# Kernel tuning notes

Measured on AMD Instinct MI355X. Metric: run time of the kernel, lower is better.

## Reference

```python
import jax, jax.numpy as jnp
import numpy as np

B, S, D_IN, E, H, WIN = 2, 4096, 512, 512, 8, 128
HD = E // H
NEG = -1e30


def setup_inputs() -> dict:
    key = jax.random.key(0)
    k0, k1, k2 = jax.random.split(key, 3)
    x = jax.random.normal(k0, (B, S, D_IN), jnp.float32)
    w_qkv = jax.random.normal(k1, (D_IN, 3 * E), jnp.float32) / np.sqrt(D_IN)
    b_qkv = jnp.zeros((3 * E,), jnp.float32)
    w_o = jax.random.normal(k2, (E, E), jnp.float32) / np.sqrt(E)
    b_o = jnp.zeros((E,), jnp.float32)
    return dict(x=x, w_qkv=w_qkv, b_qkv=b_qkv, w_o=w_o, b_o=b_o)


def _sliding_window_attn(q, k, v, w):
    # q,k,v: (B, S, H, HD). Longformer sliding-chunks: each query attends to
    # keys within +/- w positions (band of 2w+1), out-of-range masked to -inf.
    b, s, h, hd = q.shape
    assert s % (2 * w) == 0
    c = s // w  # number of width-w query chunks
    qc = q.transpose(0, 2, 1, 3).reshape(b, h, c, w, hd)  # (B,H,C,w,HD)

    def windows(t):
        # build per-chunk 3w key/value windows [c*w - w, c*w + 2w)
        t = t.transpose(0, 2, 1, 3)  # (B,H,S,HD)
        t = jnp.pad(t, ((0, 0), (0, 0), (w, w), (0, 0)))
        t = t.reshape(b, h, c + 2, w, hd)
        return jnp.concatenate([t[:, :, 0:c], t[:, :, 1:c + 1], t[:, :, 2:c + 2]], axis=3)  # (B,H,C,3w,HD)

    kc = windows(k)
    vc = windows(v)

    # chunked logits over the 3w window, scaled by sqrt(d_k)
    logits3 = jnp.einsum('bhcxd,bhcyd->bhcxy', qc, kc) / jnp.sqrt(jnp.asarray(hd, q.dtype))

    # extract diagonal band: band[x, r] = logits3[x, x + r], r in [0, 2w]
    row = jnp.arange(w)[:, None]            # (w,1)
    col = row + jnp.arange(2 * w + 1)[None, :]  # (w,2w+1), index into 3w window
    band = logits3[..., row, col]           # (B,H,C,w,2w+1)

    # mask positions outside [0, S): global key j = i + r - w
    i = (jnp.arange(c) * w)[:, None, None] + jnp.arange(w)[None, :, None]  # (C,w,1)
    j = i + (jnp.arange(2 * w + 1) - w)[None, None, :]                      # (C,w,2w+1)
    valid = (j >= 0) & (j < s)
    band = jnp.where(valid, band, NEG)

    probs = jax.nn.softmax(band, axis=-1)  # (B,H,C,w,2w+1)

    # scatter band probs back into the 3w window and contract with values
    probs3 = jnp.zeros_like(logits3).at[..., row, col].set(probs)  # (B,H,C,w,3w)
    out = jnp.einsum('bhcxy,bhcyd->bhcxd', probs3, vc)  # (B,H,C,w,HD)
    return out.reshape(b, h, s, hd).transpose(0, 2, 1, 3)  # (B,S,H,HD)


def reference(x, w_qkv, b_qkv, w_o, b_o):
    bsz, s, _ = x.shape
    qkv = x @ w_qkv + b_qkv                      # (B,S,3E)
    qkv = qkv.reshape(bsz, s, H, 3 * HD)
    q = qkv[..., :HD]
    k = qkv[..., HD:2 * HD]
    v = qkv[..., 2 * HD:]
    vals = _sliding_window_attn(q, k, v, WIN).reshape(bsz, s, E)
    return vals @ w_o + b_o
```

## Files before the change

### kernel.cpp

```cpp
#include <hip/hip_runtime.h>
#include <hip/hip_bf16.h>
#include <math.h>

typedef _Float16 f16;
typedef __attribute__((ext_vector_type(8))) _Float16 f16x8;
typedef __attribute__((ext_vector_type(4))) _Float16 f16x4;
typedef __attribute__((ext_vector_type(4))) float f32x4;

#define S_LEN 4096
#define NHEAD 8
#define HDIM 64
#define EMB 512
#define KDIM 512
#define LOG2E 1.4426950408889634f

#if __has_builtin(__builtin_amdgcn_exp2f)
#define EXP2F(x) __builtin_amdgcn_exp2f(x)
#else
#define EXP2F(x) exp2f(x)
#endif

__device__ __forceinline__ void g2l16(const void* g, void* l) {
  __builtin_amdgcn_global_load_lds(
      reinterpret_cast<const __attribute__((address_space(1))) unsigned int*>(
          reinterpret_cast<uintptr_t>(g)),
      reinterpret_cast<__attribute__((address_space(3))) unsigned int*>(
          static_cast<unsigned int>(reinterpret_cast<uintptr_t>(l))),
      16, 0, 0);
}

__global__ void cast_f32_f16_kernel(const float* __restrict__ in, f16* __restrict__ out, int n) {
  int i = (blockIdx.x * 256 + threadIdx.x) * 4;
  if (i >= n) return;
  float4 v = *(const float4*)(in + i);
  f16x4 o = { (f16)v.x, (f16)v.y, (f16)v.z, (f16)v.w };
  *(f16x4*)(out + i) = o;
}

__global__ void transpose_cast_kernel(const float* __restrict__ in, f16* __restrict__ out, int R, int C) {
  __shared__ f16 tile[64][65];
  const int c0 = blockIdx.x * 64, r0 = blockIdx.y * 64;
  const int tid = threadIdx.x;
#pragma unroll
  for (int i = 0; i < 16; ++i) {
    const int idx = i * 256 + tid;
    const int lr = idx >> 6, lc = idx & 63;
    tile[lr][lc] = (f16)in[(size_t)(r0 + lr) * C + (c0 + lc)];
  }
  __syncthreads();
#pragma unroll
  for (int i = 0; i < 16; ++i) {
    const int idx = i * 256 + tid;
    const int lc = idx >> 6, lr = idx & 63;
    out[(size_t)(c0 + lc) * R + (r0 + lr)] = tile[lr][lc];
  }
}

#define TM 128
#define TK 32

template<int MODE, int TN>
__global__ __launch_bounds__(256) void gemm_bt_kernel(
    const f16* __restrict__ A, const f16* __restrict__ Bt, const float* __restrict__ bias,
    f16* __restrict__ Qo, f16* __restrict__ Ko, f16* __restrict__ Vo,
    float* __restrict__ Co, int M, int N) {
  constexpr int JN = TN / 32;
  constexpr int BCH = TN / 64;
  __shared__ f16 As[TM][TK];
  __shared__ f16 Bs[TN][TK];
  const int m0 = blockIdx.x * TM, n0 = blockIdx.y * TN;
  const int tid = threadIdx.x;
  const int lane = tid & 63, wid = tid >> 6;
  const int wr = wid >> 1, wc = wid & 1;
  const int g = lane >> 4, q16 = lane & 15;

  const int srow = lane >> 2;
  const int skof = (lane & 3) * 8;
  const f16* Ag[2]; char* Al[2];
#pragma unroll
  for (int cb = 0; cb < 2; ++cb) {
    const int ch = wid * 2 + cb;
    Ag[cb] = A + (size_t)(m0 + ch * 16 + srow) * KDIM + skof;
    Al[cb] = (char*)As + ch * 1024;
  }
  const f16* Bg[BCH]; char* Bl[BCH];
#pragma unroll
  for (int cb = 0; cb < BCH; ++cb) {
    const int ch = wid * BCH + cb;
    Bg[cb] = Bt + (size_t)(n0 + ch * 16 + srow) * KDIM + skof;
    Bl[cb] = (char*)Bs + ch * 1024;
  }

  f32x4 zero = {0.f, 0.f, 0.f, 0.f};
  f32x4 acc[4][JN];
#pragma unroll
  for (int i = 0; i < 4; i++)
#pragma unroll
    for (int j = 0; j < JN; j++) acc[i][j] = zero;

  for (int kk = 0; kk < KDIM; kk += TK) {
    g2l16(Ag[0] + kk, Al[0]);
    g2l16(Ag[1] + kk, Al[1]);
#pragma unroll
    for (int cb = 0; cb < BCH; ++cb) g2l16(Bg[cb] + kk, Bl[cb]);
    __syncthreads();
    f16x8 af[4], bfr[JN];
#pragma unroll
    for (int i = 0; i < 4; i++) af[i] = *(const f16x8*)&As[wr * 64 + i * 16 + q16][8 * g];
#pragma unroll
    for (int j = 0; j < JN; j++) bfr[j] = *(const f16x8*)&Bs[wc * (TN / 2) + j * 16 + q16][8 * g];
#pragma unroll
    for (int i = 0; i < 4; i++)
#pragma unroll
      for (int j = 0; j < JN; j++)
        acc[i][j] = __builtin_amdgcn_mfma_f32_16x16x32_f16(af[i], bfr[j], acc[i][j], 0, 0, 0);
    __syncthreads();
  }

#pragma unroll
  for (int i = 0; i < 4; i++)
#pragma unroll
    for (int j = 0; j < JN; j++) {
      const int n = n0 + wc * (TN / 2) + j * 16 + q16;
      const float bs = bias[n];
      const int mbase = m0 + wr * 64 + i * 16 + 4 * g;
      if (MODE == 1) {
#pragma unroll
        for (int r = 0; r < 4; r++) Co[(size_t)(mbase + r) * N + n] = acc[i][j][r] + bs;
      } else {
        const int b = mbase >> 12, s = mbase & (S_LEN - 1);
        const int h = n / 192, rr = n - h * 192;
        const size_t bh = (size_t)b * NHEAD + h;
        if (rr < 64) {
#pragma unroll
          for (int r = 0; r < 4; r++)
            Qo[(bh * S_LEN + s + r) * HDIM + rr] = (f16)((acc[i][j][r] + bs) * 0.125f);
        } else if (rr < 128) {
#pragma unroll
          for (int r = 0; r < 4; r++)
            Ko[(bh * S_LEN + s + r) * HDIM + (rr - 64)] = (f16)(acc[i][j][r] + bs);
        } else {
#pragma unroll
          for (int r = 0; r < 4; r++)
            Vo[(bh * S_LEN + s + r) * HDIM + (rr - 128)] = (f16)(acc[i][j][r] + bs);
        }
      }
    }
}

#define VSOFF 40960

__global__ __launch_bounds__(256) void attn_kernel(
    const f16* __restrict__ Q, const f16* __restrict__ K,
    const f16* __restrict__ V, f16* __restrict__ O) {
  __shared__ __align__(16) char smem[81920];

  const int wg = blockIdx.x;
  const int vv = (wg & 7) * 128 + (wg >> 3);
  const int bh = vv >> 6, qc = vv & 63;
  const int b = bh >> 3, h = bh & 7;
  const int tid = threadIdx.x;
  const int wid = tid >> 6, lane = tid & 63;
  const int g = lane >> 4, q16 = lane & 15;
  const int qb = qc * 64;
  const int wb = qb - 128;
  const int qw = qb + wid * 16;
  const int qg = qw + q16;

  const f16* Kb_g = K + (size_t)bh * S_LEN * HDIM;
  const f16* Vb_g = V + (size_t)bh * S_LEN * HDIM;

#pragma unroll
  for (int rd = 0; rd < 10; ++rd) {
    const int idx = rd * 256 + tid;
    const int r = idx >> 3, sl = idx & 7;
    const int key = min(max(wb + r, 0), S_LEN - 1);
    int4 kvv = *(const int4*)(Kb_g + (size_t)key * HDIM + sl * 8);
    *(int4*)(smem + r * 128 + ((sl ^ (r & 7)) << 4)) = kvv;
  }
#pragma unroll
  for (int rd = 0; rd < 10; ++rd) {
    const int idx = rd * 256 + tid;
    const int r = idx >> 3, c8 = (idx & 7) * 8;
    const int key = min(max(wb + r, 0), S_LEN - 1);
    int4 vvv = *(const int4*)(Vb_g + (size_t)key * HDIM + c8);
    *(int4*)(smem + VSOFF + (c8 >> 4) * 10240 + (r >> 2) * 128 + (r & 3) * 32 + ((c8 & 8) << 1)) = vvv;
  }
  __syncthreads();

  const f16* Qb = Q + ((size_t)bh * S_LEN + qw) * HDIM;
  f16x8 qf0 = *(const f16x8*)(Qb + q16 * HDIM + 8 * g);
  f16x8 qf1 = *(const f16x8*)(Qb + q16 * HDIM + 32 + 8 * g);

  f32x4 zero = {0.f, 0.f, 0.f, 0.f};
  f32x4 o[4];
#pragma unroll
  for (int dt = 0; dt < 4; dt++) o[dt] = zero;
  float m_run = 0.f;
  float l_run = 0.f;

  const unsigned troff = (unsigned)(g * 128 + q16 * 8);

#pragma unroll
  for (int t = 0; t < 9; ++t) {
    const int kAp = wid * 16 + 32 * t;
    const int kBp = kAp + 16;
    const int rrA = kAp + q16;
    const int rrB = kBp + q16;
    f16x8 ka0 = *(const f16x8*)(smem + rrA * 128 + (((g    ) ^ (rrA & 7)) << 4));
    f16x8 ka1 = *(const f16x8*)(smem + rrA * 128 + (((g + 4) ^ (rrA & 7)) << 4));
    f16x8 kb0 = *(const f16x8*)(smem + rrB * 128 + (((g    ) ^ (rrB & 7)) << 4));
    f16x8 kb1 = *(const f16x8*)(smem + rrB * 128 + (((g + 4) ^ (rrB & 7)) << 4));

    f32x4 sA = zero, sB = zero;
    sA = __builtin_amdgcn_mfma_f32_16x16x32_f16(ka0, qf0, sA, 0, 0, 0);
    sA = __builtin_amdgcn_mfma_f32_16x16x32_f16(ka1, qf1, sA, 0, 0, 0);
    sB = __builtin_amdgcn_mfma_f32_16x16x32_f16(kb0, qf0, sB, 0, 0, 0);
    sB = __builtin_amdgcn_mfma_f32_16x16x32_f16(kb1, qf1, sB, 0, 0, 0);

    float sv[8];
    float mx = -INFINITY;
#pragma unroll
    for (int i = 0; i < 4; i++) {
      const int kgA = wb + kAp + 4 * g + i;
      const int kgB = wb + kBp + 4 * g + i;
      const bool okA = ((unsigned)(kgA - qg + 128) <= 256u) && ((unsigned)kgA < S_LEN);
      const bool okB = ((unsigned)(kgB - qg + 128) <= 256u) && ((unsigned)kgB < S_LEN);
      sv[i]     = okA ? sA[i] : -INFINITY;
      sv[i + 4] = okB ? sB[i] : -INFINITY;
      mx = fmaxf(mx, fmaxf(sv[i], sv[i + 4]));
    }

    float pA[4], pB[4];
#pragma unroll
    for (int i = 0; i < 4; i++) {
      pA[i] = EXP2F((sv[i] - m_run) * LOG2E);
      pB[i] = EXP2F((sv[i + 4] - m_run) * LOG2E);
    }

    if (__builtin_expect(!__all(mx - m_run <= 8.f), 0)) {
      float mxq = fmaxf(mx, __shfl_xor(mx, 16));
      mxq = fmaxf(mxq, __shfl_xor(mxq, 32));
      const float mnew = fmaxf(m_run, mxq);
      const float resc = EXP2F((m_run - mnew) * LOG2E);
#pragma unroll
      for (int i = 0; i < 4; i++) { pA[i] *= resc; pB[i] *= resc; }
      l_run *= resc;
      float ri[4];
#pragma unroll
      for (int i = 0; i < 4; i++) ri[i] = __shfl(resc, 4 * g + i);
#pragma unroll
      for (int dt = 0; dt < 4; dt++)
#pragma unroll
        for (int i = 0; i < 4; i++) o[dt][i] *= ri[i];
      m_run = mnew;
    }

    f16x4 pfA, pfB;
#pragma unroll
    for (int i = 0; i < 4; i++) {
      l_run += pA[i] + pB[i];
      pfA[i] = (f16)pA[i];
      pfB[i] = (f16)pB[i];
    }

    const int kcA = kAp;
    const int kcB = min(kBp, 304);
    f16x4 bA[4], bB[4];
#pragma unroll
    for (int dt = 0; dt < 4; ++dt) {
      unsigned aA = (unsigned)(uintptr_t)(smem + VSOFF + dt * 10240 + (kcA >> 2) * 128) + troff;
      unsigned aB = (unsigned)(uintptr_t)(smem + VSOFF + dt * 10240 + (kcB >> 2) * 128) + troff;
      asm volatile("ds_read_b64_tr_b16 %0, %1" : "=v"(bA[dt]) : "v"(aA));
      asm volatile("ds_read_b64_tr_b16 %0, %1" : "=v"(bB[dt]) : "v"(aB));
    }
    asm volatile("s_waitcnt lgkmcnt(0)" ::: "memory");
    __builtin_amdgcn_sched_barrier(0);

#pragma unroll
    for (int dt = 0; dt < 4; dt++) {
      o[dt] = __builtin_amdgcn_mfma_f32_16x16x16f16(pfA, bA[dt], o[dt], 0, 0, 0);
      o[dt] = __builtin_amdgcn_mfma_f32_16x16x16f16(pfB, bB[dt], o[dt], 0, 0, 0);
    }
  }

  l_run += __shfl_xor(l_run, 16);
  l_run += __shfl_xor(l_run, 32);
  const float linv = 1.f / l_run;
  float li[4];
#pragma unroll
  for (int i = 0; i < 4; i++) li[i] = __shfl(linv, 4 * g + i);
#pragma unroll
  for (int dt = 0; dt < 4; dt++)
#pragma unroll
    for (int i = 0; i < 4; i++) {
      const int s_idx = qw + 4 * g + i;
      O[((size_t)b * S_LEN + s_idx) * EMB + h * HDIM + dt * 16 + q16] = (f16)(o[dt][i] * li[i]);
    }
}

extern "C" void kernel_launch(void* const* d_in, const int* in_sizes, int n_in,
                              void* d_out, int out_size, void* d_ws, size_t ws_size,
                              hipStream_t stream) {
  const float* x     = (const float*)d_in[0];
  const float* w_qkv = (const float*)d_in[1];
  const float* b_qkv = (const float*)d_in[2];
  const float* w_o   = (const float*)d_in[3];
  const float* b_o   = (const float*)d_in[4];
  float* out = (float*)d_out;

  char* ws = (char*)d_ws;
  f16* xb    = (f16*)(ws);
  f16* wqkvt = (f16*)(ws + 8388608);
  f16* wot   = (f16*)(ws + 9961472);
  f16* Qs    = (f16*)(ws + 10485760);
  f16* Ks    = (f16*)(ws + 18874368);
  f16* Vs    = (f16*)(ws + 27262976);
  f16* attn  = (f16*)(ws + 35651584);

  cast_f32_f16_kernel<<<4096, 256, 0, stream>>>(x, xb, 8192 * 512);
  transpose_cast_kernel<<<dim3(24, 8), 256, 0, stream>>>(w_qkv, wqkvt, 512, 1536);
  transpose_cast_kernel<<<dim3(8, 8), 256, 0, stream>>>(w_o, wot, 512, 512);
  gemm_bt_kernel<0, 128><<<dim3(64, 12), 256, 0, stream>>>(xb, wqkvt, b_qkv, Qs, Ks, Vs,
                                                           (float*)nullptr, 8192, 1536);
  attn_kernel<<<1024, 256, 0, stream>>>(Qs, Ks, Vs, attn);
  gemm_bt_kernel<1, 64><<<dim3(64, 8), 256, 0, stream>>>(attn, wot, b_o,
                                                         (f16*)nullptr, (f16*)nullptr, (f16*)nullptr,
                                                         out, 8192, 512);
}
```

Measured before the change: 67.41 us.

## Merge prep kernels, add MFMA priority hints, vectorize attention output stores

Merges the x cast and both weight transpose-casts into one prep kernel launch that dispatches on block index, removing two kernel launches. Raises wave priority around the MFMA blocks in the attention loop to favour matrix issue. Stages the normalized attention output through shared memory so each lane writes 16-byte contiguous f16 chunks instead of scattered 2-byte stores. The staging adds a block barrier and extra LDS traffic at the end of the attention kernel.

```diff
diff --git a/kernel.cpp b/kernel.cpp
--- a/kernel.cpp
+++ b/kernel.cpp
@@ -29,18 +29,32 @@
       16, 0, 0);
 }
 
-__global__ void cast_f32_f16_kernel(const float* __restrict__ in, f16* __restrict__ out, int n) {
-  int i = (blockIdx.x * 256 + threadIdx.x) * 4;
-  if (i >= n) return;
-  float4 v = *(const float4*)(in + i);
-  f16x4 o = { (f16)v.x, (f16)v.y, (f16)v.z, (f16)v.w };
-  *(f16x4*)(out + i) = o;
-}
-
-__global__ void transpose_cast_kernel(const float* __restrict__ in, f16* __restrict__ out, int R, int C) {
+__global__ __launch_bounds__(256) void prep_kernel(
+    const float* __restrict__ x, f16* __restrict__ xb,
+    const float* __restrict__ w_qkv, f16* __restrict__ wqkvt,
+    const float* __restrict__ w_o, f16* __restrict__ wot) {
   __shared__ f16 tile[64][65];
-  const int c0 = blockIdx.x * 64, r0 = blockIdx.y * 64;
+  const int bid = blockIdx.x;
   const int tid = threadIdx.x;
+  if (bid < 4096) {
+    const int i = (bid * 256 + tid) * 4;
+    float4 v = *(const float4*)(x + i);
+    f16x4 o = { (f16)v.x, (f16)v.y, (f16)v.z, (f16)v.w };
+    *(f16x4*)(xb + i) = o;
+    return;
+  }
+  const float* in;
+  f16* out;
+  int R, C, c0, r0;
+  if (bid < 4288) {
+    const int t = bid - 4096;
+    in = w_qkv; out = wqkvt; R = 512; C = 1536;
+    c0 = (t % 24) * 64; r0 = (t / 24) * 64;
+  } else {
+    const int t = bid - 4288;
+    in = w_o; out = wot; R = 512; C = 512;
+    c0 = (t & 7) * 64; r0 = (t >> 3) * 64;
+  }
 #pragma unroll
   for (int i = 0; i < 16; ++i) {
     const int idx = i * 256 + tid;
@@ -213,10 +227,12 @@
     f16x8 kb1 = *(const f16x8*)(smem + rrB * 128 + (((g + 4) ^ (rrB & 7)) << 4));
 
     f32x4 sA = zero, sB = zero;
+    __builtin_amdgcn_s_setprio(1);
     sA = __builtin_amdgcn_mfma_f32_16x16x32_f16(ka0, qf0, sA, 0, 0, 0);
     sA = __builtin_amdgcn_mfma_f32_16x16x32_f16(ka1, qf1, sA, 0, 0, 0);
     sB = __builtin_amdgcn_mfma_f32_16x16x32_f16(kb0, qf0, sB, 0, 0, 0);
     sB = __builtin_amdgcn_mfma_f32_16x16x32_f16(kb1, qf1, sB, 0, 0, 0);
+    __builtin_amdgcn_s_setprio(0);
 
     float sv[8];
     float mx = -INFINITY;
@@ -277,11 +293,13 @@
     asm volatile("s_waitcnt lgkmcnt(0)" ::: "memory");
     __builtin_amdgcn_sched_barrier(0);
 
+    __builtin_amdgcn_s_setprio(1);
 #pragma unroll
     for (int dt = 0; dt < 4; dt++) {
       o[dt] = __builtin_amdgcn_mfma_f32_16x16x16f16(pfA, bA[dt], o[dt], 0, 0, 0);
       o[dt] = __builtin_amdgcn_mfma_f32_16x16x16f16(pfB, bB[dt], o[dt], 0, 0, 0);
     }
+    __builtin_amdgcn_s_setprio(0);
   }
 
   l_run += __shfl_xor(l_run, 16);
@@ -290,13 +308,22 @@
   float li[4];
 #pragma unroll
   for (int i = 0; i < 4; i++) li[i] = __shfl(linv, 4 * g + i);
+
+  __syncthreads();
+  float* st = (float*)smem + wid * 1024;
 #pragma unroll
   for (int dt = 0; dt < 4; dt++)
 #pragma unroll
-    for (int i = 0; i < 4; i++) {
-      const int s_idx = qw + 4 * g + i;
-      O[((size_t)b * S_LEN + s_idx) * EMB + h * HDIM + dt * 16 + q16] = (f16)(o[dt][i] * li[i]);
-    }
+    for (int i = 0; i < 4; i++)
+      st[(4 * g + i) * 64 + dt * 16 + q16] = o[dt][i] * li[i];
+  const int r = lane >> 2, c0 = (lane & 3) * 16;
+  const float* sp = st + r * 64 + c0;
+  f16x8 h0, h1;
+#pragma unroll
+  for (int j = 0; j < 8; j++) { h0[j] = (f16)sp[j]; h1[j] = (f16)sp[8 + j]; }
+  f16* dst = O + ((size_t)b * S_LEN + qw + r) * EMB + h * HDIM + c0;
+  *(f16x8*)dst = h0;
+  *(f16x8*)(dst + 8) = h1;
 }
 
 extern "C" void kernel_launch(void* const* d_in, const int* in_sizes, int n_in,
@@ -318,9 +345,7 @@
   f16* Vs    = (f16*)(ws + 27262976);
   f16* attn  = (f16*)(ws + 35651584);
 
-  cast_f32_f16_kernel<<<4096, 256, 0, stream>>>(x, xb, 8192 * 512);
-  transpose_cast_kernel<<<dim3(24, 8), 256, 0, stream>>>(w_qkv, wqkvt, 512, 1536);
-  transpose_cast_kernel<<<dim3(8, 8), 256, 0, stream>>>(w_o, wot, 512, 512);
+  prep_kernel<<<4352, 256, 0, stream>>>(x, xb, w_qkv, wqkvt, w_o, wot);
   gemm_bt_kernel<0, 128><<<dim3(64, 12), 256, 0, stream>>>(xb, wqkvt, b_qkv, Qs, Ks, Vs,
                                                            (float*)nullptr, 8192, 1536);
   attn_kernel<<<1024, 256, 0, stream>>>(Qs, Ks, Vs, attn);
```

Measured after the change: 66.62 us. No clear change (-1.2%).
